# Performance work log

Hardware: AMD Instinct MI355X
Metric: run time of the kernel (lower is better)

## Reference

```python
import jax, jax.numpy as jnp
import numpy as np

D_MODEL = 2048
N_HEADS = 16
D_HEAD = D_MODEL // N_HEADS
D_FF = 4 * D_MODEL
LN_EPS = 1e-5


def setup_inputs() -> dict:
    key = jax.random.key(0)
    ks = jax.random.split(key, 12)
    s = 1.0 / np.sqrt(D_MODEL)
    sf = 1.0 / np.sqrt(D_FF)
    return {
        "x": jax.random.normal(ks[0], (1, 2048, D_MODEL), dtype=jnp.float32),
        "ln1_g": jnp.ones((D_MODEL,), jnp.float32),
        "ln1_b": jnp.zeros((D_MODEL,), jnp.float32),
        # weights stored [in, out] (transpose of torch layout; equivalent under random init)
        "Wq": jax.random.normal(ks[1], (D_MODEL, D_MODEL), jnp.float32) * s,
        "Wk": jax.random.normal(ks[2], (D_MODEL, D_MODEL), jnp.float32) * s,
        "Wv": jax.random.normal(ks[3], (D_MODEL, D_MODEL), jnp.float32) * s,
        "Wp": jax.random.normal(ks[4], (D_MODEL, D_MODEL), jnp.float32) * s,
        "bp": jnp.zeros((D_MODEL,), jnp.float32),
        "ln2_g": jnp.ones((D_MODEL,), jnp.float32),
        "ln2_b": jnp.zeros((D_MODEL,), jnp.float32),
        "W1": jax.random.normal(ks[5], (D_MODEL, D_FF), jnp.float32) * s,
        "b1": jnp.zeros((D_FF,), jnp.float32),
        "W2": jax.random.normal(ks[6], (D_FF, D_MODEL), jnp.float32) * sf,
        "b2": jnp.zeros((D_MODEL,), jnp.float32),
    }


def _layer_norm(x, g, b):
    mu = jnp.mean(x, axis=-1, keepdims=True)
    var = jnp.mean(jnp.square(x - mu), axis=-1, keepdims=True)
    return (x - mu) * jax.lax.rsqrt(var + LN_EPS) * g + b


def _attention(h, Wq, Wk, Wv, Wp, bp):
    B, S, E = h.shape
    q = (h @ Wq).reshape(B, S, N_HEADS, D_HEAD)
    k = (h @ Wk).reshape(B, S, N_HEADS, D_HEAD)
    v = (h @ Wv).reshape(B, S, N_HEADS, D_HEAD)
    # [B, H, S, S] causal scores (matches the naive materialized original)
    scores = jnp.einsum("bqhd,bkhd->bhqk", q, k) / np.sqrt(D_HEAD).astype(np.float32)
    causal = jnp.arange(S)[:, None] >= jnp.arange(S)[None, :]
    scores = jnp.where(causal, scores, -jnp.inf)
    attn = jax.nn.softmax(scores, axis=-1)
    out = jnp.einsum("bhqk,bkhd->bqhd", attn, v).reshape(B, S, E)
    return out @ Wp + bp


def reference(x, ln1_g, ln1_b, Wq, Wk, Wv, Wp, bp, ln2_g, ln2_b, W1, b1, W2, b2):
    # attention branch: x += MHA(LN1(x)); dropout=0 (inference)
    x1 = x + _attention(_layer_norm(x, ln1_g, ln1_b), Wq, Wk, Wv, Wp, bp)
    # ff branch: FeedForward adds its own residual on the normalized input
    g = _layer_norm(x1, ln2_g, ln2_b)
    mlp = jax.nn.gelu(g @ W1 + b1, approximate=False) @ W2 + b2
    return x1 + (g + mlp)
```

## Files before the change

kernel.cpp:

```cpp
#include <hip/hip_runtime.h>
#include <math.h>

typedef unsigned int u32;
typedef unsigned short u16;
typedef __attribute__((ext_vector_type(8))) short short8;
typedef __attribute__((ext_vector_type(4))) float f32x4;

__device__ __forceinline__ u16 f2bf(float f) {
  u32 u = __builtin_bit_cast(u32, f);
  u += 0x7FFFu + ((u >> 16) & 1u);
  return (u16)(u >> 16);
}
__device__ __forceinline__ float bf2f(u16 h) {
  u32 u = ((u32)h) << 16;
  return __builtin_bit_cast(float, u);
}
__device__ __forceinline__ void gload_lds16(const void* g, void* l) {
  __builtin_amdgcn_global_load_lds((const __attribute__((address_space(1))) u32*)g,
                                   (__attribute__((address_space(3))) u32*)l, 16, 0, 0);
}
__device__ __forceinline__ f32x4 mfma16(short8 a, short8 b, f32x4 c) {
  return __builtin_amdgcn_mfma_f32_16x16x32_bf16(a, b, c, 0, 0, 0);
}

__global__ __launch_bounds__(256) void transpose_cast(const float* __restrict__ src,
                                                      u16* __restrict__ dst, int K, int N) {
  __shared__ __attribute__((aligned(16))) u16 tile[64][72];
  const int n0 = blockIdx.x * 64, k0 = blockIdx.y * 64;
  const int t = threadIdx.x;
  const int tr = t >> 4;
  const int tc4 = (t & 15) * 4;
#pragma unroll
  for (int p = 0; p < 4; ++p) {
    int row = p * 16 + tr;
    const float4 v = *(const float4*)(src + (size_t)(k0 + row) * N + n0 + tc4);
    tile[tc4 + 0][row] = f2bf(v.x);
    tile[tc4 + 1][row] = f2bf(v.y);
    tile[tc4 + 2][row] = f2bf(v.z);
    tile[tc4 + 3][row] = f2bf(v.w);
  }
  __syncthreads();
  const int nr = t >> 2;
  const int kc = (t & 3) * 16;
  u16* d = dst + (size_t)(n0 + nr) * K + k0 + kc;
  *(short8*)(d) = *(const short8*)&tile[nr][kc];
  *(short8*)(d + 8) = *(const short8*)&tile[nr][kc + 8];
}

__global__ __launch_bounds__(256) void transpose_v(const u16* __restrict__ qkv,
                                                   u16* __restrict__ vT) {
  __shared__ __attribute__((aligned(16))) u16 tile[64][72];
  const int kv0 = blockIdx.x * 64, d0 = blockIdx.y * 64, h = blockIdx.z;
  const int t = threadIdx.x;
  const int tr = t >> 3;
  const int tc8 = (t & 7) * 8;
#pragma unroll
  for (int p = 0; p < 2; ++p) {
    int row = p * 32 + tr;
    short8 v = *(const short8*)(qkv + (size_t)(kv0 + row) * 6144 + 4096 + h * 128 + d0 + tc8);
#pragma unroll
    for (int j = 0; j < 8; ++j) tile[tc8 + j][row] = (u16)v[j];
  }
  __syncthreads();
  const int dr = t >> 2;
  const int kc = (t & 3) * 16;
  u16* dst = vT + ((size_t)h * 128 + d0 + dr) * 2048 + kv0 + kc;
  *(short8*)dst = *(const short8*)&tile[dr][kc];
  *(short8*)(dst + 8) = *(const short8*)&tile[dr][kc + 8];
}

__global__ __launch_bounds__(256) void ln_kernel(const float* __restrict__ x,
                                                 const float* __restrict__ gw,
                                                 const float* __restrict__ bw,
                                                 u16* __restrict__ out) {
  const int row = blockIdx.x, t = threadIdx.x;
  const float* xr = x + (size_t)row * 2048;
  const float4 v0 = *(const float4*)(xr + t * 8);
  const float4 v1 = *(const float4*)(xr + t * 8 + 4);
  float s = v0.x + v0.y + v0.z + v0.w + v1.x + v1.y + v1.z + v1.w;
  float q = v0.x * v0.x + v0.y * v0.y + v0.z * v0.z + v0.w * v0.w +
            v1.x * v1.x + v1.y * v1.y + v1.z * v1.z + v1.w * v1.w;
#pragma unroll
  for (int w = 32; w; w >>= 1) { s += __shfl_xor(s, w); q += __shfl_xor(q, w); }
  __shared__ float rs[4], rq[4];
  const int wid = t >> 6, lane = t & 63;
  if (!lane) { rs[wid] = s; rq[wid] = q; }
  __syncthreads();
  s = rs[0] + rs[1] + rs[2] + rs[3];
  q = rq[0] + rq[1] + rq[2] + rq[3];
  const float mu = s * (1.f / 2048.f);
  const float var = q * (1.f / 2048.f) - mu * mu;
  const float rstd = rsqrtf(var + 1e-5f);
  const float4 g0 = *(const float4*)(gw + t * 8);
  const float4 g1 = *(const float4*)(gw + t * 8 + 4);
  const float4 b0 = *(const float4*)(bw + t * 8);
  const float4 b1 = *(const float4*)(bw + t * 8 + 4);
  short8 o;
  o[0] = (short)f2bf((v0.x - mu) * rstd * g0.x + b0.x);
  o[1] = (short)f2bf((v0.y - mu) * rstd * g0.y + b0.y);
  o[2] = (short)f2bf((v0.z - mu) * rstd * g0.z + b0.z);
  o[3] = (short)f2bf((v0.w - mu) * rstd * g0.w + b0.w);
  o[4] = (short)f2bf((v1.x - mu) * rstd * g1.x + b1.x);
  o[5] = (short)f2bf((v1.y - mu) * rstd * g1.y + b1.y);
  o[6] = (short)f2bf((v1.z - mu) * rstd * g1.z + b1.z);
  o[7] = (short)f2bf((v1.w - mu) * rstd * g1.w + b1.w);
  *(short8*)(out + (size_t)row * 2048 + t * 8) = o;
}

template <int EPI>
__global__ __launch_bounds__(512, 2) void gemm2(const u16* __restrict__ A,
                                                const u16* __restrict__ Bt,
                                                int M, int N, int K, int Kc,
                                                u16* __restrict__ outB,
                                                const float* __restrict__ bias,
                                                float* __restrict__ pA) {
  __shared__ __attribute__((aligned(16))) u16 lds[3 * 24576];
  const int m0 = blockIdx.y * 256, n0 = blockIdx.x * 128;
  const int tid = threadIdx.x, wid = tid >> 6, lane = tid & 63;
  const int wr = wid >> 1, wc = wid & 1;
  const int lq = lane & 15, lk = lane >> 4;
  const int kStart = blockIdx.z * Kc;
  const int NT = Kc / 64;

  size_t aoff[4], boff[2];
#pragma unroll
  for (int s = 0; s < 4; ++s) {
    int c = s * 512 + tid;
    int row = c >> 3, col = ((c & 7) ^ (row & 7)) * 8;
    aoff[s] = (size_t)(m0 + row) * K + col;
  }
#pragma unroll
  for (int s = 0; s < 2; ++s) {
    int c = s * 512 + tid;
    int row = c >> 3, col = ((c & 7) ^ (row & 7)) * 8;
    boff[s] = (size_t)(n0 + row) * K + col;
  }
  const int dstc = wid * 512 + lane * 8;

#define STAGE_A(s, t2) \
  gload_lds16(A + aoff[s] + (size_t)(kStart + (t2) * 64), \
              lds + ((t2) % 3) * 24576 + (s) * 4096 + dstc)
#define STAGE_B(s, t2) \
  gload_lds16(Bt + boff[s] + (size_t)(kStart + (t2) * 64), \
              lds + ((t2) % 3) * 24576 + 16384 + (s) * 4096 + dstc)

  STAGE_A(0, 0); STAGE_A(1, 0); STAGE_A(2, 0); STAGE_A(3, 0); STAGE_B(0, 0); STAGE_B(1, 0);
  STAGE_A(0, 1); STAGE_A(1, 1); STAGE_A(2, 1); STAGE_A(3, 1); STAGE_B(0, 1); STAGE_B(1, 1);
  asm volatile("s_waitcnt vmcnt(6)" ::: "memory");
  __builtin_amdgcn_s_barrier();
  __builtin_amdgcn_sched_barrier(0);

  f32x4 acc[4][4] = {};
  int cur = 0;
  for (int t = 0; t < NT; ++t) {
    const char* bufA = (const char*)lds + cur * 49152;
    const char* bufB = bufA + 32768;
    const int t2 = t + 2;
    const bool st = t2 < NT;
    const int xorq = (lq & 7) << 4;
#pragma unroll
    for (int ph = 0; ph < 2; ++ph) {
      short8 af[4], bf[4];
#pragma unroll
      for (int mi = 0; mi < 4; ++mi) {
        int ar = wr * 64 + mi * 16 + lq;
        af[mi] = *(const short8*)(bufA + ar * 128 + ((ph * 64 + lk * 16) ^ xorq));
      }
#pragma unroll
      for (int ni = 0; ni < 4; ++ni) {
        int br = wc * 64 + ni * 16 + lq;
        bf[ni] = *(const short8*)(bufB + br * 128 + ((ph * 64 + lk * 16) ^ xorq));
      }
      if (st) {
        if (ph == 0) { STAGE_A(0, t2); STAGE_A(1, t2); STAGE_A(2, t2); }
        else         { STAGE_A(3, t2); STAGE_B(0, t2); STAGE_B(1, t2); }
      }
      __builtin_amdgcn_s_barrier();
      __builtin_amdgcn_s_setprio(1);
#pragma unroll
      for (int mi = 0; mi < 4; ++mi)
#pragma unroll
        for (int ni = 0; ni < 4; ++ni)
          acc[mi][ni] = mfma16(af[mi], bf[ni], acc[mi][ni]);
      __builtin_amdgcn_s_setprio(0);
      if (ph == 1) {
        if (st) asm volatile("s_waitcnt vmcnt(6)" ::: "memory");
        else    asm volatile("s_waitcnt vmcnt(0)" ::: "memory");
      }
      __builtin_amdgcn_s_barrier();
      __builtin_amdgcn_sched_barrier(0);
    }
    cur = (cur == 2) ? 0 : cur + 1;
  }
#undef STAGE_A
#undef STAGE_B

  float* pp = nullptr;
  if (EPI == 4) pp = pA + (size_t)blockIdx.z * ((size_t)M * N);
#pragma unroll
  for (int mi = 0; mi < 4; ++mi) {
#pragma unroll
    for (int ni = 0; ni < 4; ++ni) {
      const int col = n0 + wc * 64 + ni * 16 + lq;
#pragma unroll
      for (int r = 0; r < 4; ++r) {
        const int row = m0 + wr * 64 + mi * 16 + lk * 4 + r;
        const size_t idx = (size_t)row * N + col;
        float v = acc[mi][ni][r];
        if (EPI == 0) {
          outB[idx] = f2bf(v);
        } else if (EPI == 2) {
          float xg = v + bias[col];
          outB[idx] = f2bf(0.5f * xg * (1.f + erff(xg * 0.70710678118654752f)));
        } else {
          pp[idx] = v;
        }
      }
    }
  }
}

template <int RES2>
__global__ __launch_bounds__(256) void reduce_kernel(const float* __restrict__ pA,
                                                     const float* __restrict__ bias,
                                                     const float* __restrict__ res1,
                                                     const u16* __restrict__ res2,
                                                     float* __restrict__ out,
                                                     int MN, int N) {
  const int i = (blockIdx.x * 256 + threadIdx.x) * 4;
  if (i >= MN) return;
  float4 s = *(const float4*)(pA + i);
  {
    const float4 t = *(const float4*)(pA + MN + i);
    s.x += t.x; s.y += t.y; s.z += t.z; s.w += t.w;
  }
  const int col = i & (N - 1);
  const float4 bv = *(const float4*)(bias + col);
  const float4 r1 = *(const float4*)(res1 + i);
  float4 o;
  o.x = s.x + bv.x + r1.x;
  o.y = s.y + bv.y + r1.y;
  o.z = s.z + bv.z + r1.z;
  o.w = s.w + bv.w + r1.w;
  if (RES2) {
    const u16* r2 = res2 + i;
    o.x += bf2f(r2[0]); o.y += bf2f(r2[1]); o.z += bf2f(r2[2]); o.w += bf2f(r2[3]);
  }
  *(float4*)(out + i) = o;
}

__global__ __launch_bounds__(256) void attn_kernel(const u16* __restrict__ qkv,
                                                   const u16* __restrict__ vT,
                                                   u16* __restrict__ attnout) {
  __shared__ __attribute__((aligned(16))) u16 lsK[64 * 128];
  __shared__ __attribute__((aligned(16))) u16 lsV[128 * 64];
  __shared__ __attribute__((aligned(16))) u16 lsP[4][16 * 64];
  const int h = blockIdx.x;
  const int qi = 31 - blockIdx.y;
  const int qb = qi * 64;
  const int tid = threadIdx.x, wid = tid >> 6, lane = tid & 63;
  const int lq = lane & 15, lk = lane >> 4;
  const int qw = qb + wid * 16;

  short8 qf[4];
  {
    const u16* qp = qkv + (size_t)(qw + lq) * 6144 + h * 128;
#pragma unroll
    for (int ks = 0; ks < 4; ++ks) qf[ks] = *(const short8*)(qp + ks * 32 + lk * 8);
  }
  float mreg[4], lreg[4];
  f32x4 o[8];
#pragma unroll
  for (int r = 0; r < 4; ++r) { mreg[r] = -INFINITY; lreg[r] = 0.f; }
#pragma unroll
  for (int dt = 0; dt < 8; ++dt) o[dt] = (f32x4){0.f, 0.f, 0.f, 0.f};

  const int rK = lane >> 4, sK = lane & 15;
  const int rV = lane >> 3, sV = lane & 7;
  const int nkt = qi + 1;
  for (int kt = 0; kt < nkt; ++kt) {
    const int kv0 = kt * 64;
    if (kt) __syncthreads();
#pragma unroll
    for (int i = 0; i < 4; ++i) {
      int c = wid * 4 + i;
      int rowK = c * 4 + rK;
      gload_lds16(qkv + (size_t)(kv0 + rowK) * 6144 + 2048 + h * 128 + ((sK ^ (rowK & 7)) * 8),
                  lsK + c * 512);
      int rowV = c * 8 + rV;
      gload_lds16(vT + ((size_t)h * 128 + rowV) * 2048 + kv0 + ((sV ^ (rowV & 7)) * 8),
                  lsV + c * 512);
    }
    __syncthreads();

    f32x4 sc[4];
#pragma unroll
    for (int nt = 0; nt < 4; ++nt) sc[nt] = (f32x4){0.f, 0.f, 0.f, 0.f};
#pragma unroll
    for (int ks = 0; ks < 4; ++ks) {
#pragma unroll
      for (int nt = 0; nt < 4; ++nt) {
        int kvr = nt * 16 + lq;
        short8 kf = *(const short8*)((const char*)lsK + kvr * 256 +
                                     ((ks * 64 + lk * 16) ^ ((kvr & 7) << 4)));
        sc[nt] = mfma16(qf[ks], kf, sc[nt]);
      }
    }
    float rmax[4] = {-INFINITY, -INFINITY, -INFINITY, -INFINITY};
#pragma unroll
    for (int nt = 0; nt < 4; ++nt) {
      int kv = kv0 + nt * 16 + lq;
#pragma unroll
      for (int r = 0; r < 4; ++r) {
        int qrow = qw + lk * 4 + r;
        float s = (kv <= qrow) ? sc[nt][r] * 0.08838834764831845f : -INFINITY;
        sc[nt][r] = s;
        rmax[r] = fmaxf(rmax[r], s);
      }
    }
#pragma unroll
    for (int r = 0; r < 4; ++r)
#pragma unroll
      for (int w = 1; w < 16; w <<= 1) rmax[r] = fmaxf(rmax[r], __shfl_xor(rmax[r], w));
    bool grow = false;
#pragma unroll
    for (int r = 0; r < 4; ++r) grow |= (rmax[r] > mreg[r] + 8.f);
    if (__any(grow)) {
#pragma unroll
      for (int r = 0; r < 4; ++r) {
        float mn = fmaxf(mreg[r], rmax[r]);
        float alpha = __expf(mreg[r] - mn);
        mreg[r] = mn;
        lreg[r] *= alpha;
#pragma unroll
        for (int dt = 0; dt < 8; ++dt) o[dt][r] *= alpha;
      }
    }
    float rsum[4] = {0.f, 0.f, 0.f, 0.f};
    u16* P = &lsP[wid][0];
#pragma unroll
    for (int nt = 0; nt < 4; ++nt) {
#pragma unroll
      for (int r = 0; r < 4; ++r) {
        float p = __expf(sc[nt][r] - mreg[r]);
        rsum[r] += p;
        int prow = lk * 4 + r, pcol = nt * 16 + lq;
        *(u16*)((char*)P + prow * 128 + ((pcol * 2) ^ ((prow & 7) << 4))) = f2bf(p);
      }
    }
#pragma unroll
    for (int r = 0; r < 4; ++r) {
#pragma unroll
      for (int w = 1; w < 16; w <<= 1) rsum[r] += __shfl_xor(rsum[r], w);
      lreg[r] += rsum[r];
    }
#pragma unroll
    for (int kk = 0; kk < 2; ++kk) {
      short8 pa = *(const short8*)((const char*)P + lq * 128 +
                                   ((kk * 64 + lk * 16) ^ ((lq & 7) << 4)));
#pragma unroll
      for (int dt = 0; dt < 8; ++dt) {
        int dr = dt * 16 + lq;
        short8 vf = *(const short8*)((const char*)lsV + dr * 128 +
                                     ((kk * 64 + lk * 16) ^ ((dr & 7) << 4)));
        o[dt] = mfma16(pa, vf, o[dt]);
      }
    }
  }
#pragma unroll
  for (int r = 0; r < 4; ++r) {
    float inv = 1.f / lreg[r];
    int row = qw + lk * 4 + r;
    u16* op = attnout + (size_t)row * 2048 + h * 128 + lq;
#pragma unroll
    for (int dt = 0; dt < 8; ++dt) op[dt * 16] = f2bf(o[dt][r] * inv);
  }
}

extern "C" void kernel_launch(void* const* d_in, const int* in_sizes, int n_in,
                              void* d_out, int out_size, void* d_ws, size_t ws_size,
                              hipStream_t stream) {
  (void)in_sizes; (void)n_in; (void)out_size; (void)ws_size;
  const float* x    = (const float*)d_in[0];
  const float* ln1g = (const float*)d_in[1];
  const float* ln1b = (const float*)d_in[2];
  const float* Wq   = (const float*)d_in[3];
  const float* Wk   = (const float*)d_in[4];
  const float* Wv   = (const float*)d_in[5];
  const float* Wp   = (const float*)d_in[6];
  const float* bp   = (const float*)d_in[7];
  const float* ln2g = (const float*)d_in[8];
  const float* ln2b = (const float*)d_in[9];
  const float* W1   = (const float*)d_in[10];
  const float* b1   = (const float*)d_in[11];
  const float* W2   = (const float*)d_in[12];
  const float* b2   = (const float*)d_in[13];
  float* out = (float*)d_out;
  char* ws = (char*)d_ws;

  u16* wqkvT = (u16*)(ws + 0);
  u16* hbuf  = (u16*)(ws + 25165824);
  u16* wpT   = (u16*)(ws + 33554432);
  u16* w1T   = (u16*)(ws + 41943040);
  u16* w2T   = (u16*)(ws + 75497472);
  u16* qkv   = (u16*)(ws + 109051904);
  u16* vT    = (u16*)(ws + 134217728);
  u16* attn  = (u16*)(ws + 142606336);
  float* x1  = (float*)(ws + 150994944);
  u16* g     = (u16*)(ws + 167772160);
  u16* ff1   = (u16*)(ws + 0);
  float* projP = (float*)(ws + 109051904);
  float* ffP = (float*)(ws + 33554432);

  dim3 b256(256), b512(512);
  transpose_cast<<<dim3(32, 32), b256, 0, stream>>>(Wq, wqkvT, 2048, 2048);
  transpose_cast<<<dim3(32, 32), b256, 0, stream>>>(Wk, wqkvT + 2048 * 2048, 2048, 2048);
  transpose_cast<<<dim3(32, 32), b256, 0, stream>>>(Wv, wqkvT + 4096 * 2048, 2048, 2048);
  transpose_cast<<<dim3(32, 32), b256, 0, stream>>>(Wp, wpT, 2048, 2048);
  transpose_cast<<<dim3(128, 32), b256, 0, stream>>>(W1, w1T, 2048, 8192);
  transpose_cast<<<dim3(32, 128), b256, 0, stream>>>(W2, w2T, 8192, 2048);
  ln_kernel<<<2048, b256, 0, stream>>>(x, ln1g, ln1b, hbuf);
  gemm2<0><<<dim3(48, 8, 1), b512, 0, stream>>>(hbuf, wqkvT, 2048, 6144, 2048, 2048,
                                                qkv, nullptr, nullptr);
  transpose_v<<<dim3(32, 2, 16), b256, 0, stream>>>(qkv, vT);
  attn_kernel<<<dim3(16, 32), b256, 0, stream>>>(qkv, vT, attn);
  gemm2<4><<<dim3(16, 8, 2), b512, 0, stream>>>(attn, wpT, 2048, 2048, 2048, 1024,
                                                nullptr, nullptr, projP);
  reduce_kernel<0><<<4096, b256, 0, stream>>>(projP, bp, x, nullptr, x1, 4194304, 2048);
  ln_kernel<<<2048, b256, 0, stream>>>(x1, ln2g, ln2b, g);
  gemm2<2><<<dim3(64, 8, 1), b512, 0, stream>>>(g, w1T, 2048, 8192, 2048, 2048,
                                                ff1, b1, nullptr);
  gemm2<4><<<dim3(16, 8, 2), b512, 0, stream>>>(ff1, w2T, 2048, 2048, 8192, 4096,
                                                nullptr, nullptr, ffP);
  reduce_kernel<1><<<4096, b256, 0, stream>>>(ffP, b2, x1, g, out, 4194304, 2048);
}
```

Measured before the change: 434.8 us.

## Switch GEMMs to 256x256 tiles with K=32 stages and 4-way split-K

Result: faster. 423.8 us (-2.5%).

```diff
diff --git a/kernel.cpp b/kernel.cpp
--- a/kernel.cpp
+++ b/kernel.cpp
@@ -108,103 +108,102 @@
 }
 
 template <int EPI>
-__global__ __launch_bounds__(512, 2) void gemm2(const u16* __restrict__ A,
+__global__ __launch_bounds__(512, 2) void gemm3(const u16* __restrict__ A,
                                                 const u16* __restrict__ Bt,
                                                 int M, int N, int K, int Kc,
                                                 u16* __restrict__ outB,
                                                 const float* __restrict__ bias,
-                                                float* __restrict__ pA) {
-  __shared__ __attribute__((aligned(16))) u16 lds[3 * 24576];
-  const int m0 = blockIdx.y * 256, n0 = blockIdx.x * 128;
+                                                float* __restrict__ pA,
+                                                float* __restrict__ pB) {
+  __shared__ __attribute__((aligned(16))) u16 lds[3 * 16384];
+  const int m0 = blockIdx.y * 256, n0 = blockIdx.x * 256;
   const int tid = threadIdx.x, wid = tid >> 6, lane = tid & 63;
-  const int wr = wid >> 1, wc = wid & 1;
+  const int wr = wid >> 2, wc = wid & 3;
   const int lq = lane & 15, lk = lane >> 4;
   const int kStart = blockIdx.z * Kc;
-  const int NT = Kc / 64;
-
-  size_t aoff[4], boff[2];
-#pragma unroll
-  for (int s = 0; s < 4; ++s) {
-    int c = s * 512 + tid;
-    int row = c >> 3, col = ((c & 7) ^ (row & 7)) * 8;
-    aoff[s] = (size_t)(m0 + row) * K + col;
-  }
+  const int NT = Kc / 32;
+
+  size_t aoff[2], boff[2];
 #pragma unroll
   for (int s = 0; s < 2; ++s) {
     int c = s * 512 + tid;
-    int row = c >> 3, col = ((c & 7) ^ (row & 7)) * 8;
-    boff[s] = (size_t)(n0 + row) * K + col;
-  }
-  const int dstc = wid * 512 + lane * 8;
-
-#define STAGE_A(s, t2) \
-  gload_lds16(A + aoff[s] + (size_t)(kStart + (t2) * 64), \
-              lds + ((t2) % 3) * 24576 + (s) * 4096 + dstc)
-#define STAGE_B(s, t2) \
-  gload_lds16(Bt + boff[s] + (size_t)(kStart + (t2) * 64), \
-              lds + ((t2) % 3) * 24576 + 16384 + (s) * 4096 + dstc)
-
-  STAGE_A(0, 0); STAGE_A(1, 0); STAGE_A(2, 0); STAGE_A(3, 0); STAGE_B(0, 0); STAGE_B(1, 0);
-  STAGE_A(0, 1); STAGE_A(1, 1); STAGE_A(2, 1); STAGE_A(3, 1); STAGE_B(0, 1); STAGE_B(1, 1);
-  asm volatile("s_waitcnt vmcnt(6)" ::: "memory");
+    int row = c >> 2;
+    int col = ((c & 3) ^ ((row >> 1) & 3)) * 8;
+    aoff[s] = (size_t)(m0 + row) * K + kStart + col;
+    boff[s] = (size_t)(n0 + row) * K + kStart + col;
+  }
+  u16* ldst = lds + tid * 8;
+
+#define STA(s, buf, t2) gload_lds16(A + aoff[s] + (size_t)((t2) * 32), \
+                                    ldst + (buf) * 16384 + (s) * 4096)
+#define STB(s, buf, t2) gload_lds16(Bt + boff[s] + (size_t)((t2) * 32), \
+                                    ldst + (buf) * 16384 + 8192 + (s) * 4096)
+
+  STA(0, 0, 0); STA(1, 0, 0); STB(0, 0, 0); STB(1, 0, 0);
+  STA(0, 1, 1); STA(1, 1, 1); STB(0, 1, 1); STB(1, 1, 1);
+  asm volatile("s_waitcnt vmcnt(4)" ::: "memory");
   __builtin_amdgcn_s_barrier();
   __builtin_amdgcn_sched_barrier(0);
 
-  f32x4 acc[4][4] = {};
-  int cur = 0;
+  f32x4 acc[8][4] = {};
+  int cur = 0, nxt2 = 2;
   for (int t = 0; t < NT; ++t) {
-    const char* bufA = (const char*)lds + cur * 49152;
-    const char* bufB = bufA + 32768;
-    const int t2 = t + 2;
-    const bool st = t2 < NT;
-    const int xorq = (lq & 7) << 4;
-#pragma unroll
-    for (int ph = 0; ph < 2; ++ph) {
-      short8 af[4], bf[4];
-#pragma unroll
-      for (int mi = 0; mi < 4; ++mi) {
-        int ar = wr * 64 + mi * 16 + lq;
-        af[mi] = *(const short8*)(bufA + ar * 128 + ((ph * 64 + lk * 16) ^ xorq));
-      }
-#pragma unroll
-      for (int ni = 0; ni < 4; ++ni) {
-        int br = wc * 64 + ni * 16 + lq;
-        bf[ni] = *(const short8*)(bufB + br * 128 + ((ph * 64 + lk * 16) ^ xorq));
-      }
-      if (st) {
-        if (ph == 0) { STAGE_A(0, t2); STAGE_A(1, t2); STAGE_A(2, t2); }
-        else         { STAGE_A(3, t2); STAGE_B(0, t2); STAGE_B(1, t2); }
-      }
-      __builtin_amdgcn_s_barrier();
-      __builtin_amdgcn_s_setprio(1);
-#pragma unroll
-      for (int mi = 0; mi < 4; ++mi)
-#pragma unroll
-        for (int ni = 0; ni < 4; ++ni)
-          acc[mi][ni] = mfma16(af[mi], bf[ni], acc[mi][ni]);
-      __builtin_amdgcn_s_setprio(0);
-      if (ph == 1) {
-        if (st) asm volatile("s_waitcnt vmcnt(6)" ::: "memory");
-        else    asm volatile("s_waitcnt vmcnt(0)" ::: "memory");
-      }
-      __builtin_amdgcn_s_barrier();
-      __builtin_amdgcn_sched_barrier(0);
-    }
+    const char* bufc = (const char*)lds + cur * 32768;
+    const bool st = (t + 2) < NT;
+    short8 bf[4], af[4];
+#pragma unroll
+    for (int ni = 0; ni < 4; ++ni) {
+      int br = wc * 64 + ni * 16 + lq;
+      bf[ni] = *(const short8*)(bufc + 16384 + br * 64 + ((lk ^ ((br >> 1) & 3)) << 4));
+    }
+#pragma unroll
+    for (int mi = 0; mi < 4; ++mi) {
+      int ar = wr * 128 + mi * 16 + lq;
+      af[mi] = *(const short8*)(bufc + ar * 64 + ((lk ^ ((ar >> 1) & 3)) << 4));
+    }
+    if (st) { STA(0, nxt2, t + 2); STA(1, nxt2, t + 2); }
+    __builtin_amdgcn_s_setprio(1);
+#pragma unroll
+    for (int mi = 0; mi < 4; ++mi)
+#pragma unroll
+      for (int ni = 0; ni < 4; ++ni)
+        acc[mi][ni] = mfma16(af[mi], bf[ni], acc[mi][ni]);
+    __builtin_amdgcn_s_setprio(0);
+#pragma unroll
+    for (int mi = 0; mi < 4; ++mi) {
+      int ar = wr * 128 + (mi + 4) * 16 + lq;
+      af[mi] = *(const short8*)(bufc + ar * 64 + ((lk ^ ((ar >> 1) & 3)) << 4));
+    }
+    if (st) { STB(0, nxt2, t + 2); STB(1, nxt2, t + 2); }
+    __builtin_amdgcn_s_setprio(1);
+#pragma unroll
+    for (int mi = 0; mi < 4; ++mi)
+#pragma unroll
+      for (int ni = 0; ni < 4; ++ni)
+        acc[mi + 4][ni] = mfma16(af[mi], bf[ni], acc[mi + 4][ni]);
+    __builtin_amdgcn_s_setprio(0);
+    if (st) asm volatile("s_waitcnt vmcnt(4)" ::: "memory");
+    else    asm volatile("s_waitcnt vmcnt(0)" ::: "memory");
+    __builtin_amdgcn_s_barrier();
+    __builtin_amdgcn_sched_barrier(0);
     cur = (cur == 2) ? 0 : cur + 1;
-  }
-#undef STAGE_A
-#undef STAGE_B
+    nxt2 = (nxt2 == 2) ? 0 : nxt2 + 1;
+  }
+#undef STA
+#undef STB
 
   float* pp = nullptr;
-  if (EPI == 4) pp = pA + (size_t)blockIdx.z * ((size_t)M * N);
-#pragma unroll
-  for (int mi = 0; mi < 4; ++mi) {
+  if (EPI == 4) {
+    pp = (blockIdx.z < 2 ? pA : pB) + (size_t)(blockIdx.z & 1) * ((size_t)M * N);
+  }
+#pragma unroll
+  for (int mi = 0; mi < 8; ++mi) {
 #pragma unroll
     for (int ni = 0; ni < 4; ++ni) {
       const int col = n0 + wc * 64 + ni * 16 + lq;
 #pragma unroll
       for (int r = 0; r < 4; ++r) {
-        const int row = m0 + wr * 64 + mi * 16 + lk * 4 + r;
+        const int row = m0 + wr * 128 + mi * 16 + lk * 4 + r;
         const size_t idx = (size_t)row * N + col;
         float v = acc[mi][ni][r];
         if (EPI == 0) {
@@ -220,8 +219,9 @@
   }
 }
 
-template <int RES2>
+template <int NS, int RES2>
 __global__ __launch_bounds__(256) void reduce_kernel(const float* __restrict__ pA,
+                                                     const float* __restrict__ pB,
                                                      const float* __restrict__ bias,
                                                      const float* __restrict__ res1,
                                                      const u16* __restrict__ res2,
@@ -233,6 +233,11 @@
   {
     const float4 t = *(const float4*)(pA + MN + i);
     s.x += t.x; s.y += t.y; s.z += t.z; s.w += t.w;
+  }
+  if (NS == 4) {
+    const float4 t0 = *(const float4*)(pB + i);
+    const float4 t1 = *(const float4*)(pB + MN + i);
+    s.x += t0.x + t1.x; s.y += t0.y + t1.y; s.z += t0.z + t1.z; s.w += t0.w + t1.w;
   }
   const int col = i & (N - 1);
   const float4 bv = *(const float4*)(bias + col);
@@ -409,8 +414,10 @@
   float* x1  = (float*)(ws + 150994944);
   u16* g     = (u16*)(ws + 167772160);
   u16* ff1   = (u16*)(ws + 0);
-  float* projP = (float*)(ws + 109051904);
-  float* ffP = (float*)(ws + 33554432);
+  float* projPA = (float*)(ws + 0);
+  float* projPB = (float*)(ws + 109051904);
+  float* ffPA = (float*)(ws + 33554432);
+  float* ffPB = (float*)(ws + 109051904);
 
   dim3 b256(256), b512(512);
   transpose_cast<<<dim3(32, 32), b256, 0, stream>>>(Wq, wqkvT, 2048, 2048);
@@ -420,17 +427,19 @@
   transpose_cast<<<dim3(128, 32), b256, 0, stream>>>(W1, w1T, 2048, 8192);
   transpose_cast<<<dim3(32, 128), b256, 0, stream>>>(W2, w2T, 8192, 2048);
   ln_kernel<<<2048, b256, 0, stream>>>(x, ln1g, ln1b, hbuf);
-  gemm2<0><<<dim3(48, 8, 1), b512, 0, stream>>>(hbuf, wqkvT, 2048, 6144, 2048, 2048,
-                                                qkv, nullptr, nullptr);
+  gemm3<0><<<dim3(24, 8, 1), b512, 0, stream>>>(hbuf, wqkvT, 2048, 6144, 2048, 2048,
+                                                qkv, nullptr, nullptr, nullptr);
   transpose_v<<<dim3(32, 2, 16), b256, 0, stream>>>(qkv, vT);
   attn_kernel<<<dim3(16, 32), b256, 0, stream>>>(qkv, vT, attn);
-  gemm2<4><<<dim3(16, 8, 2), b512, 0, stream>>>(attn, wpT, 2048, 2048, 2048, 1024,
-                                                nullptr, nullptr, projP);
-  reduce_kernel<0><<<4096, b256, 0, stream>>>(projP, bp, x, nullptr, x1, 4194304, 2048);
+  gemm3<4><<<dim3(8, 8, 4), b512, 0, stream>>>(attn, wpT, 2048, 2048, 2048, 512,
+                                               nullptr, nullptr, projPA, projPB);
+  reduce_kernel<4, 0><<<4096, b256, 0, stream>>>(projPA, projPB, bp, x, nullptr, x1,
+                                                 4194304, 2048);
   ln_kernel<<<2048, b256, 0, stream>>>(x1, ln2g, ln2b, g);
-  gemm2<2><<<dim3(64, 8, 1), b512, 0, stream>>>(g, w1T, 2048, 8192, 2048, 2048,
-                                                ff1, b1, nullptr);
-  gemm2<4><<<dim3(16, 8, 2), b512, 0, stream>>>(ff1, w2T, 2048, 2048, 8192, 4096,
-                                                nullptr, nullptr, ffP);
-  reduce_kernel<1><<<4096, b256, 0, stream>>>(ffP, b2, x1, g, out, 4194304, 2048);
-}
+  gemm3<2><<<dim3(32, 8, 1), b512, 0, stream>>>(g, w1T, 2048, 8192, 2048, 2048,
+                                                ff1, b1, nullptr, nullptr);
+  gemm3<4><<<dim3(8, 8, 4), b512, 0, stream>>>(ff1, w2T, 2048, 2048, 8192, 2048,
+                                               nullptr, nullptr, ffPA, ffPB);
+  reduce_kernel<4, 1><<<4096, b256, 0, stream>>>(ffPA, ffPB, b2, x1, g, out,
+                                                 4194304, 2048);
+}
```
